# Kernel optimization log

Measured on AMD Instinct MI355X. Metric: run time of the kernel, lower is better.

Reference implementation:

```python
import jax, jax.numpy as jnp
import numpy as np

_SAMPLING_EPS = 1e-5
B, V = 256, 128000


def _apply_min_p(logits, min_p):
    # probs >= min_p * max_prob  <=>  keep; else logit -> -inf
    probs = jax.nn.softmax(logits, axis=-1)
    max_probs = jnp.max(probs, axis=-1, keepdims=True)
    keep = probs >= (min_p[:, None] * max_probs)
    return jnp.where(keep, logits, -jnp.inf)


def _apply_top_k_top_p(logits, top_k, top_p):
    # Sort ascending once; derive per-row keep-thresholds for both filters.
    logits_sort = jnp.sort(logits, axis=-1)  # [B, V] ascending
    # top-k threshold: value at position V-k (kth largest)
    k_idx = jnp.clip(V - top_k, 0, V - 1).astype(jnp.int32)
    k_thresh = jnp.take_along_axis(logits_sort, k_idx[:, None], axis=-1)  # [B,1]
    # top-p: on ascending-sorted probs, token is kept iff cumsum > 1 - p
    probs_sort = jax.nn.softmax(logits_sort, axis=-1)
    probs_cum = jnp.cumsum(probs_sort, axis=-1)
    kept = probs_cum > (1.0 - top_p[:, None])
    kept = kept.at[:, -1].set(True)  # always keep the max-prob token
    p_thresh = jnp.min(jnp.where(kept, logits_sort, jnp.inf), axis=-1, keepdims=True)
    thresh = jnp.maximum(k_thresh, p_thresh)
    return jnp.where(logits >= thresh, logits, -jnp.inf)


def setup_inputs() -> dict:
    key = jax.random.key(0)
    k1, k2, k3, k4, k5 = jax.random.split(key, 5)
    logits = jax.random.normal(k1, (B, V), jnp.float32)
    temperature = jax.random.uniform(k2, (B,), jnp.float32, 0.1, 1.5)
    temperature = temperature.at[:8].set(0.0)  # greedy rows
    min_p = jax.random.uniform(k3, (B,), jnp.float32, 0.0, 0.2)
    top_k = jax.random.randint(k4, (B,), 1, 64).astype(jnp.int32)
    top_p = jax.random.uniform(k5, (B,), jnp.float32, 0.5, 1.0)
    return {"logits": logits, "temperature": temperature, "min_p": min_p,
            "top_k": top_k, "top_p": top_p}


def reference(logits, temperature, min_p, top_k, top_p):
    logits = logits.astype(jnp.float32)
    greedy = jnp.argmax(logits, axis=-1)  # [B]
    # safe temperature divide (greedy rows have temp ~ 0 but are overridden)
    safe_t = jnp.where(temperature < _SAMPLING_EPS, 1.0, temperature)
    scaled = logits / safe_t[:, None]
    scaled = _apply_min_p(scaled, min_p)
    masked = _apply_top_k_top_p(scaled, top_k, top_p)
    # Gumbel-max trick == categorical sampling from softmax(masked)
    u = jax.random.uniform(jax.random.key(42), masked.shape, jnp.float32, 1e-10, 1.0)
    gumbel = -jnp.log(-jnp.log(u))
    random_sampled = jnp.argmax(masked + gumbel, axis=-1)
    sampled = jnp.where(temperature < _SAMPLING_EPS, greedy, random_sampled)
    return sampled[:, None]  # sampled_token_ids [B, 1]
```

## Files before the change

kernel.cpp:

```cpp
#include <hip/hip_runtime.h>
#include <stdint.h>

typedef unsigned long long u64;
typedef unsigned int u32;

#define VOCAB 128000
#define NV4   32000
#define NROWS 256
#define BLK   1024
#define NW    16
#define NB    4096
#define CAPL  4096
#define SEPS  1e-5f
#define FIXS  17592186044416.0

__device__ __forceinline__ u32 f2key(float f){
  u32 u = __float_as_uint(f);
  return (u & 0x80000000u) ? ~u : (u | 0x80000000u);
}
__device__ __forceinline__ float key2f(u32 k){
  u32 u = (k & 0x80000000u) ? (k ^ 0x80000000u) : ~k;
  return __uint_as_float(u);
}
__device__ __forceinline__ u64 efix(float e){
  return (u64)((double)e * FIXS);
}

__device__ __forceinline__ void tf2x32(u32 x0, u32 x1, u32 &o0, u32 &o1){
  const u32 k0 = 0u, k1 = 42u, k2 = 0u ^ 42u ^ 0x1BD11BDAu;
  x0 += k0; x1 += k1;
#define TFR(r) { x0 += x1; x1 = (x1 << (r)) | (x1 >> (32 - (r))); x1 ^= x0; }
  TFR(13) TFR(15) TFR(26) TFR(6)
  x0 += k1; x1 += k2 + 1u;
  TFR(17) TFR(29) TFR(16) TFR(24)
  x0 += k2; x1 += k0 + 2u;
  TFR(13) TFR(15) TFR(26) TFR(6)
  x0 += k0; x1 += k1 + 3u;
  TFR(17) TFR(29) TFR(16) TFR(24)
  x0 += k1; x1 += k2 + 4u;
  TFR(13) TFR(15) TFR(26) TFR(6)
  x0 += k2; x1 += k0 + 5u;
#undef TFR
  o0 = x0; o1 = x1;
}
__device__ __forceinline__ u32 gumbel_bits(u32 i){
  u32 o0, o1; tf2x32(0u, i, o0, o1);
  return o0 ^ o1;
}
__device__ __forceinline__ float bits2gumbel(u32 b){
  float f = __uint_as_float(0x3F800000u | (b >> 9)) - 1.0f;
  float u = fmaxf(1e-10f, f + 1e-10f);
  return -logf(-logf(u));
}

__device__ __forceinline__ void cross4096_u32(
    const u32* arr, u32* aux, u32 target, u32* out_idx, u32* out_before, int t)
{
  aux[t] = arr[4*t+0] + arr[4*t+1] + arr[4*t+2] + arr[4*t+3];
  __syncthreads();
  if (t < 64){
    u32 gs = 0u;
    #pragma unroll
    for (int j=0;j<16;j++) gs += aux[t*16+j];
    u32 pref = gs;
    #pragma unroll
    for (int d=1; d<64; d<<=1){ u32 v = __shfl_up(pref, d, 64); if (t >= d) pref += v; }
    u64 bal = __ballot(pref > target);
    int g = bal ? (__ffsll((long long)bal) - 1) : 63;
    u32 pg = __shfl(pref, g, 64);
    u32 gg = __shfl(gs, g, 64);
    if (t == 0){
      u32 c = pg - gg;
      u32 idx = (u32)(g*64 + 63);
      for (int j=0;j<16;j++){
        u32 v = aux[g*16+j];
        if (c + v > target){
          int base = (g*16+j)*4;
          for (int q=0;q<4;q++){
            u32 w = arr[base+q];
            if (c + w > target){ idx = (u32)(base+q); goto doneu; }
            c += w;
          }
        }
        c += v;
      }
      doneu:
      *out_idx = idx; *out_before = c;
    }
  }
}

__device__ __forceinline__ void cross4096_u64(
    const u64* arr, u64* aux, u64 target, u32* out_idx, u64* out_before, int t)
{
  aux[t] = arr[4*t+0] + arr[4*t+1] + arr[4*t+2] + arr[4*t+3];
  __syncthreads();
  if (t < 64){
    u64 gs = 0ull;
    #pragma unroll
    for (int j=0;j<16;j++) gs += aux[t*16+j];
    u64 pref = gs;
    #pragma unroll
    for (int d=1; d<64; d<<=1){
      u64 v = __shfl_up((unsigned long long)pref, d, 64); if (t >= d) pref += v;
    }
    u64 bal = __ballot(pref > target);
    int g = bal ? (__ffsll((long long)bal) - 1) : 63;
    u64 pg = __shfl((unsigned long long)pref, g, 64);
    u64 gg = __shfl((unsigned long long)gs, g, 64);
    if (t == 0){
      u64 c = pg - gg;
      u32 idx = (u32)(g*64 + 63);
      for (int j=0;j<16;j++){
        u64 v = aux[g*16+j];
        if (c + v > target){
          int base = (g*16+j)*4;
          for (int q=0;q<4;q++){
            u64 w = arr[base+q];
            if (c + w > target){ idx = (u32)(base+q); goto donev; }
            c += w;
          }
        }
        c += v;
      }
      donev:
      *out_idx = idx; *out_before = c;
    }
  }
}

__device__ __forceinline__ void cross4096_mass(
    const u64* arr, u64* aux, float topp_v, u64* out_target,
    u32* out_idx, u64* out_before, int t)
{
  aux[t] = arr[4*t+0] + arr[4*t+1] + arr[4*t+2] + arr[4*t+3];
  __syncthreads();
  if (t < 64){
    u64 gs = 0ull;
    #pragma unroll
    for (int j=0;j<16;j++) gs += aux[t*16+j];
    u64 pref = gs;
    #pragma unroll
    for (int d=1; d<64; d<<=1){
      u64 v = __shfl_up((unsigned long long)pref, d, 64); if (t >= d) pref += v;
    }
    u64 total = __shfl((unsigned long long)pref, 63, 64);
    u64 target = (u64)((double)(1.0f - topp_v) * (double)total);
    u64 bal = __ballot(pref > target);
    int g = bal ? (__ffsll((long long)bal) - 1) : 63;
    u64 pg = __shfl((unsigned long long)pref, g, 64);
    u64 gg = __shfl((unsigned long long)gs, g, 64);
    if (t == 0){
      u64 c = pg - gg;
      u32 idx = (u32)(g*64 + 63);
      for (int j=0;j<16;j++){
        u64 v = aux[g*16+j];
        if (c + v > target){
          int base = (g*16+j)*4;
          for (int q=0;q<4;q++){
            u64 w = arr[base+q];
            if (c + w > target){ idx = (u32)(base+q); goto donem; }
            c += w;
          }
        }
        c += v;
      }
      donem:
      *out_target = target; *out_idx = idx; *out_before = c;
    }
  }
}

__device__ __forceinline__ void cross256_u32(const u32* arr, u32 target, u32* out_idx, int t){
  if (t < 64){
    u32 gs = arr[4*t+0]+arr[4*t+1]+arr[4*t+2]+arr[4*t+3];
    u32 pref = gs;
    #pragma unroll
    for (int d=1; d<64; d<<=1){ u32 v=__shfl_up(pref,d,64); if (t>=d) pref+=v; }
    u64 bal = __ballot(pref > target);
    int g = bal ? (__ffsll((long long)bal)-1) : 63;
    u32 pg=__shfl(pref,g,64), gg=__shfl(gs,g,64);
    if (t==0){
      u32 c = pg-gg; u32 idx=(u32)(g*4+3);
      for (int q=0;q<4;q++){ u32 w=arr[g*4+q]; if (c+w>target){ idx=(u32)(g*4+q); break; } c+=w; }
      *out_idx = idx;
    }
  }
}
__device__ __forceinline__ void cross256_u64(const u64* arr, u64 target, u32* out_idx, int t){
  if (t < 64){
    u64 gs = arr[4*t+0]+arr[4*t+1]+arr[4*t+2]+arr[4*t+3];
    u64 pref = gs;
    #pragma unroll
    for (int d=1; d<64; d<<=1){
      u64 v=__shfl_up((unsigned long long)pref,d,64); if (t>=d) pref+=v;
    }
    u64 bal = __ballot(pref > target);
    int g = bal ? (__ffsll((long long)bal)-1) : 63;
    u64 pg=__shfl((unsigned long long)pref,g,64), gg=__shfl((unsigned long long)gs,g,64);
    if (t==0){
      u64 c = pg-gg; u32 idx=(u32)(g*4+3);
      for (int q=0;q<4;q++){ u64 w=arr[g*4+q]; if (c+w>target){ idx=(u32)(g*4+q); break; } c+=w; }
      *out_idx = idx;
    }
  }
}

__device__ __forceinline__ void msmerge(float &m1, float &S1, float m2, float S2){
  float mm = fmaxf(m1, m2);
  if (mm == -INFINITY){ m1 = mm; S1 = 0.0f; return; }
  S1 = S1*__expf(m1-mm) + S2*__expf(m2-mm);
  m1 = mm;
}

__device__ __forceinline__ void argmax_write(
    float best, u32 bi, float* wrf, u32* wru, int ln, int wv, int b, int* out)
{
  #pragma unroll
  for (int d=32; d>0; d>>=1){
    float c2=__shfl_down(best,d,64); u32 i2=__shfl_down(bi,d,64);
    if (c2>best || (c2==best && i2<bi)){best=c2;bi=i2;}
  }
  if (ln==0){ wrf[wv]=best; wru[wv]=bi; }
  __syncthreads();
  if (wv==0){
    float b1=(ln<NW)?wrf[ln]:-INFINITY; u32 i1=(ln<NW)?wru[ln]:0xFFFFFFFFu;
    #pragma unroll
    for (int d=32; d>0; d>>=1){
      float b2=__shfl_down(b1,d,64); u32 i2=__shfl_down(i1,d,64);
      if (b2>b1 || (b2==b1 && i2<i1)){b1=b2;i1=i2;}
    }
    if (ln==0) out[b]=(int)i1;
  }
}

__global__ __launch_bounds__(BLK) void k_all(
    const float* __restrict__ logits, const float* __restrict__ temp,
    const float* __restrict__ minp, const int* __restrict__ topk,
    const float* __restrict__ topp, int* __restrict__ out)
{
  __shared__ u32 cnt[NB];
  __shared__ u64 mass[NB];
  __shared__ u64 aux64[BLK];
  __shared__ u64 list[CAPL];
  __shared__ float wrf1[NW], wrf2[NW];
  __shared__ u32  wru1[NW];
  __shared__ float sh_m;
  __shared__ u32 sh_lstar, sh_K, sh_len, sh_acc1, sh_acc2;
  __shared__ u32 sh_idx, sh_bef32;
  __shared__ u64 sh_bef64, sh_tfix;

  u32* aux32 = (u32*)aux64;

  const int b = blockIdx.x;
  const int t = threadIdx.x;
  const int ln = t & 63, wv = t >> 6;
  const float T = temp[b];
  const float* row = logits + (size_t)b * VOCAB;
  const float4* row4 = (const float4*)row;

  if (T < SEPS){
    float M = -INFINITY; u32 Mi = 0xFFFFFFFFu;
    for (int i=t; i<NV4; i+=BLK){
      float4 q = row4[i];
      #pragma unroll
      for (int j=0;j<4;j++){
        float l = (&q.x)[j]; u32 gi = (u32)(i*4+j);
        if (l > M){ M = l; Mi = gi; }
      }
    }
    argmax_write(M, Mi, wrf1, wru1, ln, wv, b, out);
    return;
  }

  const float invT = 1.0f / T;
  for (int i=t;i<NB;i+=BLK) cnt[i]=0u;
  if (t==0){ sh_K=0u; sh_len=0u; sh_acc1=0u; sh_acc2=0u; }
  __syncthreads();
  float ms = -INFINITY, S = 0.0f;
  for (int i=t; i<NV4; i+=2*BLK){
    float4 qa = row4[i];
    int i2 = i + BLK;
    bool h2 = (i2 < NV4);
    float4 qb;
    if (h2) qb = row4[i2];
    #pragma unroll
    for (int j=0;j<4;j++){
      float l = (&qa.x)[j];
      float s = l * invT;
      if (s > ms){ S = S*__expf(ms - s) + 1.0f; ms = s; }
      else       { S += __expf(s - ms); }
      atomicAdd(&cnt[f2key(l)>>20], 1u);
    }
    if (h2){
      #pragma unroll
      for (int j=0;j<4;j++){
        float l = (&qb.x)[j];
        float s = l * invT;
        if (s > ms){ S = S*__expf(ms - s) + 1.0f; ms = s; }
        else       { S += __expf(s - ms); }
        atomicAdd(&cnt[f2key(l)>>20], 1u);
      }
    }
  }
  #pragma unroll
  for (int d=32; d>0; d>>=1){
    float m2 = __shfl_down(ms, d, 64); float S2 = __shfl_down(S, d, 64);
    msmerge(ms, S, m2, S2);
  }
  if (ln==0){ wrf1[wv]=ms; wrf2[wv]=S; }
  __syncthreads();
  if (wv==0){
    float m1 = (ln<NW)? wrf1[ln] : -INFINITY;
    float S1 = (ln<NW)? wrf2[ln] : 0.0f;
    #pragma unroll
    for (int d=32; d>0; d>>=1){
      float m2 = __shfl_down(m1, d, 64); float S2 = __shfl_down(S1, d, 64);
      msmerge(m1, S1, m2, S2);
    }
    if (ln==0){ sh_m = m1; wrf2[0] = S1; }
  }
  __syncthreads();
  const float m = sh_m, Z = wrf2[0];

  int tk = topk[b]; if (tk < 1) tk = 1; if (tk > VOCAB) tk = VOCAB;
  cross4096_u32(cnt, aux32, (u32)(VOCAB - tk), &sh_idx, &sh_bef32, t);
  __syncthreads();
  const u32 b1k = sh_idx;
  const u32 r1  = (u32)(VOCAB - tk + 1) - sh_bef32;

  if (t==0){
    float rhs = minp[b] * (1.0f / Z);
    u32 lo = 0u, hi = 0xFF800000u;
    while (lo < hi){
      u32 mid = lo + ((hi - lo) >> 1);
      float e = __expf(key2f(mid) * invT - m);
      if ((e / Z) >= rhs) hi = mid; else lo = mid + 1u;
    }
    sh_lstar = lo;
  }
  __syncthreads();
  const u32 lstar = sh_lstar;
  const u32 bl = lstar >> 20;

  {
    u32 pa=0u, pc=0u;
    for (int i=t;i<NB;i+=BLK){
      u32 c = cnt[i];
      if ((u32)i > bl)   pa += c;
      if ((u32)i >= b1k) pc += c;
    }
    #pragma unroll
    for (int d=32; d>0; d>>=1){ pa += __shfl_down(pa,d,64); pc += __shfl_down(pc,d,64); }
    if (ln==0){ atomicAdd(&sh_acc1, pa); atomicAdd(&sh_acc2, pc); }
  }
  __syncthreads();
  const u32 Kmin  = sh_acc1;
  const u32 cntbl = cnt[bl];
  const bool kcert = (Kmin >= (u32)tk);
  const u32 CLB = kcert ? b1k : bl;
  const u32 listlen = kcert ? sh_acc2 : (Kmin + cntbl);
  const bool fastOK = (listlen <= (u32)CAPL);

  for (int i=t;i<NB;i+=BLK) mass[i]=0ull;
  __syncthreads();
  u32 kc = 0u;
  for (int i=t; i<NV4; i+=2*BLK){
    float4 qa = row4[i];
    int i2 = i + BLK;
    bool h2 = (i2 < NV4);
    float4 qb;
    if (h2) qb = row4[i2];
    #pragma unroll
    for (int j=0;j<4;j++){
      float l = (&qa.x)[j];
      u32 key = f2key(l);
      if (key >= lstar){
        kc++;
        atomicAdd(&mass[key>>20], efix(__expf(l*invT - m)));
      }
      if (fastOK && (key>>20) >= CLB){
        u32 p = atomicAdd(&sh_len, 1u);
        list[p] = ((u64)key << 32) | (u64)(u32)(i*4+j);
      }
    }
    if (h2){
      #pragma unroll
      for (int j=0;j<4;j++){
        float l = (&qb.x)[j];
        u32 key = f2key(l);
        if (key >= lstar){
          kc++;
          atomicAdd(&mass[key>>20], efix(__expf(l*invT - m)));
        }
        if (fastOK && (key>>20) >= CLB){
          u32 p = atomicAdd(&sh_len, 1u);
          list[p] = ((u64)key << 32) | (u64)(u32)(i2*4+j);
        }
      }
    }
  }
  #pragma unroll
  for (int d=32; d>0; d>>=1) kc += __shfl_down(kc, d, 64);
  if (ln==0) atomicAdd(&sh_K, kc);
  __syncthreads();
  const u32 K = sh_K;
  const bool kval = (K >= (u32)tk);
  cross4096_mass(mass, aux64, topp[b], &sh_tfix, &sh_idx, &sh_bef64, t);
  __syncthreads();
  const u32 b1p = sh_idx;
  const u64 t1  = sh_tfix - sh_bef64;
  const u32 llen = sh_len;
  const bool needK = kval && (b1p <= b1k);
  const bool needP = (!kval) || (b1p >= b1k);

  u32 kkey = 0u, pkey = 0u;

  if (fastOK){
    if (needK){
      for (int i=t;i<NB;i+=BLK) cnt[i]=0u;
      __syncthreads();
      for (u32 i=t; i<llen; i+=BLK){
        u32 key = (u32)(list[i]>>32);
        if ((key>>20) == b1k) atomicAdd(&cnt[(key>>8)&0xFFFu], 1u);
      }
      __syncthreads();
      cross4096_u32(cnt, aux32, r1-1u, &sh_idx, &sh_bef32, t);
      __syncthreads();
      u32 b2k = sh_idx, r2 = r1 - sh_bef32;
      u32 prefk = (b1k<<12) | b2k;
      for (int i=t;i<256;i+=BLK) cnt[i]=0u;
      __syncthreads();
      for (u32 i=t; i<llen; i+=BLK){
        u32 key = (u32)(list[i]>>32);
        if ((key>>8) == prefk) atomicAdd(&cnt[key&0xFFu], 1u);
      }
      __syncthreads();
      cross256_u32(cnt, r2-1u, &sh_idx, t);
      __syncthreads();
      kkey = (prefk<<8) | sh_idx;
    }
    if (needP){
      for (int i=t;i<NB;i+=BLK) mass[i]=0ull;
      __syncthreads();
      for (u32 i=t; i<llen; i+=BLK){
        u32 key = (u32)(list[i]>>32);
        if ((key>>20) == b1p && key >= lstar)
          atomicAdd(&mass[(key>>8)&0xFFFu], efix(__expf(key2f(key)*invT - m)));
      }
      __syncthreads();
      cross4096_u64(mass, aux64, t1, &sh_idx, &sh_bef64, t);
      __syncthreads();
      u32 b2p = sh_idx; u64 t2 = t1 - sh_bef64;
      u32 prefp = (b1p<<12) | b2p;
      for (int i=t;i<256;i+=BLK) mass[i]=0ull;
      __syncthreads();
      for (u32 i=t; i<llen; i+=BLK){
        u32 key = (u32)(list[i]>>32);
        if ((key>>8) == prefp && key >= lstar)
          atomicAdd(&mass[key&0xFFu], efix(__expf(key2f(key)*invT - m)));
      }
      __syncthreads();
      cross256_u64(mass, t2, &sh_idx, t);
      __syncthreads();
      pkey = (prefp<<8) | sh_idx;
    }
    const u32 thrkey = kkey > pkey ? kkey : pkey;

    float best = -INFINITY; u32 bi = 0xFFFFFFFFu;
    for (u32 i=t; i<llen; i+=BLK){
      u64 e = list[i];
      u32 key = (u32)(e>>32);
      if (key >= thrkey){
        u32 idx = (u32)e;
        u32 c = (u32)b * (u32)VOCAB + idx;
        float cand = key2f(key)*invT + bits2gumbel(gumbel_bits(c));
        if (cand > best || (cand == best && idx < bi)){ best = cand; bi = idx; }
      }
    }
    argmax_write(best, bi, wrf1, wru1, ln, wv, b, out);
    return;
  }

  for (int i=t;i<NB;i+=BLK){ cnt[i]=0u; mass[i]=0ull; }
  __syncthreads();
  for (int i=t; i<NV4; i+=BLK){
    float4 q = row4[i];
    #pragma unroll
    for (int j=0;j<4;j++){
      float l = (&q.x)[j]; u32 key = f2key(l); u32 hi = key>>20;
      if (kval && hi == b1k) atomicAdd(&cnt[(key>>8)&0xFFFu], 1u);
      if (hi == b1p && key >= lstar)
        atomicAdd(&mass[(key>>8)&0xFFFu], efix(__expf(l*invT - m)));
    }
  }
  __syncthreads();
  cross4096_u32(cnt, aux32, r1-1u, &sh_idx, &sh_bef32, t);
  __syncthreads();
  u32 b2k = sh_idx, r2 = r1 - sh_bef32;
  cross4096_u64(mass, aux64, t1, &sh_idx, &sh_bef64, t);
  __syncthreads();
  u32 b2p = sh_idx; u64 t2 = t1 - sh_bef64;
  for (int i=t;i<256;i+=BLK){ cnt[i]=0u; mass[i]=0ull; }
  __syncthreads();
  for (int i=t; i<NV4; i+=BLK){
    float4 q = row4[i];
    #pragma unroll
    for (int j=0;j<4;j++){
      float l = (&q.x)[j]; u32 key = f2key(l);
      if (kval && (key>>8)==(((b1k<<12)|b2k)))
        atomicAdd(&cnt[key&0xFFu], 1u);
      if ((key>>8)==(((b1p<<12)|b2p)) && key >= lstar)
        atomicAdd(&mass[key&0xFFu], efix(__expf(l*invT - m)));
    }
  }
  __syncthreads();
  cross256_u32(cnt, r2-1u, &sh_idx, t);
  __syncthreads();
  if (kval) kkey = (b1k<<20)|(b2k<<8)|sh_idx;
  cross256_u64(mass, t2, &sh_idx, t);
  __syncthreads();
  pkey = (b1p<<20)|(b2p<<8)|sh_idx;
  const float thrf = key2f(kkey > pkey ? kkey : pkey);

  float best = -INFINITY; u32 bi = 0xFFFFFFFFu;
  for (int i=t; i<NV4; i+=BLK){
    float4 q = row4[i];
    #pragma unroll
    for (int j=0;j<4;j++){
      float l = (&q.x)[j];
      if (l >= thrf){
        u32 idx = (u32)(i*4+j);
        u32 c = (u32)b * (u32)VOCAB + idx;
        float cand = l*invT + bits2gumbel(gumbel_bits(c));
        if (cand > best || (cand == best && idx < bi)){ best = cand; bi = idx; }
      }
    }
  }
  argmax_write(best, bi, wrf1, wru1, ln, wv, b, out);
}

extern "C" void kernel_launch(void* const* d_in, const int* in_sizes, int n_in,
                              void* d_out, int out_size, void* d_ws, size_t ws_size,
                              hipStream_t stream)
{
  const float* logits = (const float*)d_in[0];
  const float* temp   = (const float*)d_in[1];
  const float* minp   = (const float*)d_in[2];
  const int*   topk   = (const int*)d_in[3];
  const float* topp   = (const float*)d_in[4];
  int* out = (int*)d_out;

  hipLaunchKernelGGL(k_all, dim3(NROWS), dim3(BLK), 0, stream,
                     logits, temp, minp, topk, topp, out);
}
```

Measured before the change: 63.93 us.

## Compute per-bucket exp mass in first pass and drop online softmax

The first pass now tracks only the row max, and per top bucket it accumulates exp mass measured relative to each bucket's lower edge. The global normalizer Z and the kept mass are then rebuilt in double precision by rescaling each bucket with exp(edge*invT - m). This removes the online-softmax rescaling and the second full mass histogram in the middle pass, which now only accumulates mass for the boundary bucket. It adds a second 64-bit shared atomic in the first pass plus several tree reductions. It also risks precision differences from the per-bucket fixed-point scaling.

```diff
diff --git a/kernel.cpp b/kernel.cpp
--- a/kernel.cpp
+++ b/kernel.cpp
@@ -1,5 +1,6 @@
 #include <hip/hip_runtime.h>
 #include <stdint.h>
+#include <math.h>
 
 typedef unsigned long long u64;
 typedef unsigned int u32;
@@ -12,7 +13,6 @@
 #define NB    4096
 #define CAPL  4096
 #define SEPS  1e-5f
-#define FIXS  17592186044416.0
 
 __device__ __forceinline__ u32 f2key(float f){
   u32 u = __float_as_uint(f);
@@ -22,8 +22,12 @@
   u32 u = (k & 0x80000000u) ? (k ^ 0x80000000u) : ~k;
   return __uint_as_float(u);
 }
-__device__ __forceinline__ u64 efix(float e){
-  return (u64)((double)e * FIXS);
+__device__ __forceinline__ u64 localm(float l, float edge, float invT){
+  return (u64)(__expf((l - edge) * invT) * 1.099511627776e12f);
+}
+__device__ __forceinline__ double scaleb(u32 b, double invTd, double md){
+  double e = (double)key2f(b << 20);
+  return exp(e * invTd - md) * 9.094947017729282e-13;
 }
 
 __device__ __forceinline__ void tf2x32(u32 x0, u32 x1, u32 &o0, u32 &o1){
@@ -129,44 +133,41 @@
   }
 }
 
-__device__ __forceinline__ void cross4096_mass(
-    const u64* arr, u64* aux, float topp_v, u64* out_target,
-    u32* out_idx, u64* out_before, int t)
+__device__ __forceinline__ void cross4096_f64(
+    const double* arr, double* aux, double target, u32* out_idx, double* out_before, int t)
 {
   aux[t] = arr[4*t+0] + arr[4*t+1] + arr[4*t+2] + arr[4*t+3];
   __syncthreads();
   if (t < 64){
-    u64 gs = 0ull;
+    double gs = 0.0;
     #pragma unroll
     for (int j=0;j<16;j++) gs += aux[t*16+j];
-    u64 pref = gs;
+    double pref = gs;
     #pragma unroll
     for (int d=1; d<64; d<<=1){
-      u64 v = __shfl_up((unsigned long long)pref, d, 64); if (t >= d) pref += v;
-    }
-    u64 total = __shfl((unsigned long long)pref, 63, 64);
-    u64 target = (u64)((double)(1.0f - topp_v) * (double)total);
+      double v = __shfl_up(pref, d, 64); if (t >= d) pref += v;
+    }
     u64 bal = __ballot(pref > target);
     int g = bal ? (__ffsll((long long)bal) - 1) : 63;
-    u64 pg = __shfl((unsigned long long)pref, g, 64);
-    u64 gg = __shfl((unsigned long long)gs, g, 64);
+    double pg = __shfl(pref, g, 64);
+    double gg = __shfl(gs, g, 64);
     if (t == 0){
-      u64 c = pg - gg;
+      double c = pg - gg;
       u32 idx = (u32)(g*64 + 63);
       for (int j=0;j<16;j++){
-        u64 v = aux[g*16+j];
+        double v = aux[g*16+j];
         if (c + v > target){
           int base = (g*16+j)*4;
           for (int q=0;q<4;q++){
-            u64 w = arr[base+q];
-            if (c + w > target){ idx = (u32)(base+q); goto donem; }
+            double w = arr[base+q];
+            if (c + w > target){ idx = (u32)(base+q); goto donef; }
             c += w;
           }
         }
         c += v;
       }
-      donem:
-      *out_target = target; *out_idx = idx; *out_before = c;
+      donef:
+      *out_idx = idx; *out_before = c;
     }
   }
 }
@@ -206,13 +207,6 @@
   }
 }
 
-__device__ __forceinline__ void msmerge(float &m1, float &S1, float m2, float S2){
-  float mm = fmaxf(m1, m2);
-  if (mm == -INFINITY){ m1 = mm; S1 = 0.0f; return; }
-  S1 = S1*__expf(m1-mm) + S2*__expf(m2-mm);
-  m1 = mm;
-}
-
 __device__ __forceinline__ void argmax_write(
     float best, u32 bi, float* wrf, u32* wru, int ln, int wv, int b, int* out)
 {
@@ -240,17 +234,20 @@
     const float* __restrict__ topp, int* __restrict__ out)
 {
   __shared__ u32 cnt[NB];
-  __shared__ u64 mass[NB];
+  __shared__ u64 lmass[NB];
+  __shared__ u64 list[CAPL];
   __shared__ u64 aux64[BLK];
-  __shared__ u64 list[CAPL];
-  __shared__ float wrf1[NW], wrf2[NW];
-  __shared__ u32  wru1[NW];
-  __shared__ float sh_m;
-  __shared__ u32 sh_lstar, sh_K, sh_len, sh_acc1, sh_acc2;
-  __shared__ u32 sh_idx, sh_bef32;
-  __shared__ u64 sh_bef64, sh_tfix;
+  __shared__ float wrf[NW];
+  __shared__ u32  wru[NW];
+  __shared__ u64  wrull[NW];
+  __shared__ float sh_maxL, sh_Z32;
+  __shared__ u32 sh_lstar, sh_len, sh_idx, sh_bef32, sh_u1, sh_u2;
+  __shared__ u64 sh_bef64, sh_km;
+  __shared__ double sh_befd, sh_Md;
 
   u32* aux32 = (u32*)aux64;
+  double* auxd = (double*)aux64;
+  double* absd = (double*)lmass;
 
   const int b = blockIdx.x;
   const int t = threadIdx.x;
@@ -269,59 +266,68 @@
         if (l > M){ M = l; Mi = gi; }
       }
     }
-    argmax_write(M, Mi, wrf1, wru1, ln, wv, b, out);
+    argmax_write(M, Mi, wrf, wru, ln, wv, b, out);
     return;
   }
 
   const float invT = 1.0f / T;
-  for (int i=t;i<NB;i+=BLK) cnt[i]=0u;
-  if (t==0){ sh_K=0u; sh_len=0u; sh_acc1=0u; sh_acc2=0u; }
-  __syncthreads();
-  float ms = -INFINITY, S = 0.0f;
-  for (int i=t; i<NV4; i+=2*BLK){
-    float4 qa = row4[i];
-    int i2 = i + BLK;
-    bool h2 = (i2 < NV4);
-    float4 qb;
-    if (h2) qb = row4[i2];
-    #pragma unroll
-    for (int j=0;j<4;j++){
-      float l = (&qa.x)[j];
-      float s = l * invT;
-      if (s > ms){ S = S*__expf(ms - s) + 1.0f; ms = s; }
-      else       { S += __expf(s - ms); }
-      atomicAdd(&cnt[f2key(l)>>20], 1u);
-    }
-    if (h2){
+
+  for (int i=t;i<NB;i+=BLK){ cnt[i]=0u; lmass[i]=0ull; }
+  if (t==0){ sh_len = 0u; }
+  __syncthreads();
+  {
+    float mx = -INFINITY;
+    for (int i=t; i<NV4; i+=2*BLK){
+      float4 qa = row4[i];
+      int i2 = i + BLK; bool h2 = (i2 < NV4);
+      float4 qb; if (h2) qb = row4[i2];
       #pragma unroll
       for (int j=0;j<4;j++){
-        float l = (&qb.x)[j];
-        float s = l * invT;
-        if (s > ms){ S = S*__expf(ms - s) + 1.0f; ms = s; }
-        else       { S += __expf(s - ms); }
-        atomicAdd(&cnt[f2key(l)>>20], 1u);
-      }
-    }
-  }
-  #pragma unroll
-  for (int d=32; d>0; d>>=1){
-    float m2 = __shfl_down(ms, d, 64); float S2 = __shfl_down(S, d, 64);
-    msmerge(ms, S, m2, S2);
-  }
-  if (ln==0){ wrf1[wv]=ms; wrf2[wv]=S; }
-  __syncthreads();
-  if (wv==0){
-    float m1 = (ln<NW)? wrf1[ln] : -INFINITY;
-    float S1 = (ln<NW)? wrf2[ln] : 0.0f;
-    #pragma unroll
-    for (int d=32; d>0; d>>=1){
-      float m2 = __shfl_down(m1, d, 64); float S2 = __shfl_down(S1, d, 64);
-      msmerge(m1, S1, m2, S2);
-    }
-    if (ln==0){ sh_m = m1; wrf2[0] = S1; }
-  }
-  __syncthreads();
-  const float m = sh_m, Z = wrf2[0];
+        float l = (&qa.x)[j];
+        mx = fmaxf(mx, l);
+        u32 key = f2key(l); u32 bk = key >> 20;
+        atomicAdd(&cnt[bk], 1u);
+        atomicAdd(&lmass[bk], localm(l, key2f(bk<<20), invT));
+      }
+      if (h2){
+        #pragma unroll
+        for (int j=0;j<4;j++){
+          float l = (&qb.x)[j];
+          mx = fmaxf(mx, l);
+          u32 key = f2key(l); u32 bk = key >> 20;
+          atomicAdd(&cnt[bk], 1u);
+          atomicAdd(&lmass[bk], localm(l, key2f(bk<<20), invT));
+        }
+      }
+    }
+    #pragma unroll
+    for (int d=32; d>0; d>>=1) mx = fmaxf(mx, __shfl_down(mx, d, 64));
+    if (ln==0) wrf[wv] = mx;
+    __syncthreads();
+    if (t==0){
+      float m1 = wrf[0];
+      for (int w=1; w<NW; w++) m1 = fmaxf(m1, wrf[w]);
+      sh_maxL = m1;
+    }
+  }
+  __syncthreads();
+  const float m = sh_maxL * invT;
+  const double invTd = (double)invT, md = (double)m;
+
+  for (int i0=t*4; i0<(t+1)*4; i0++){
+    u64 lm = lmass[i0];
+    double a = lm ? ((double)lm * scaleb((u32)i0, invTd, md)) : 0.0;
+    absd[i0] = a;
+  }
+  __syncthreads();
+  {
+    double s = absd[4*t+0]+absd[4*t+1]+absd[4*t+2]+absd[4*t+3];
+    auxd[t] = s; __syncthreads();
+    for (int off=512; off>0; off>>=1){ if (t<off) auxd[t] += auxd[t+off]; __syncthreads(); }
+    if (t==0) sh_Z32 = (float)auxd[0];
+    __syncthreads();
+  }
+  const float Z = sh_Z32;
 
   int tk = topk[b]; if (tk < 1) tk = 1; if (tk > VOCAB) tk = VOCAB;
   cross4096_u32(cnt, aux32, (u32)(VOCAB - tk), &sh_idx, &sh_bef32, t);
@@ -344,75 +350,96 @@
   const u32 bl = lstar >> 20;
 
   {
-    u32 pa=0u, pc=0u;
-    for (int i=t;i<NB;i+=BLK){
-      u32 c = cnt[i];
-      if ((u32)i > bl)   pa += c;
-      if ((u32)i >= b1k) pc += c;
-    }
-    #pragma unroll
-    for (int d=32; d>0; d>>=1){ pa += __shfl_down(pa,d,64); pc += __shfl_down(pc,d,64); }
-    if (ln==0){ atomicAdd(&sh_acc1, pa); atomicAdd(&sh_acc2, pc); }
-  }
-  __syncthreads();
-  const u32 Kmin  = sh_acc1;
-  const u32 cntbl = cnt[bl];
+    u32 pa = 0u;
+    for (int i=t;i<NB;i+=BLK) if ((u32)i > bl) pa += cnt[i];
+    aux32[t] = pa; __syncthreads();
+    for (int off=512; off>0; off>>=1){ if (t<off) aux32[t] += aux32[t+off]; __syncthreads(); }
+    if (t==0) sh_u1 = aux32[0];
+    __syncthreads();
+  }
+  const u32 Kmin = sh_u1;
   const bool kcert = (Kmin >= (u32)tk);
   const u32 CLB = kcert ? b1k : bl;
-  const u32 listlen = kcert ? sh_acc2 : (Kmin + cntbl);
+  {
+    u32 pa = 0u;
+    for (int i=t;i<NB;i+=BLK) if ((u32)i >= CLB) pa += cnt[i];
+    aux32[t] = pa; __syncthreads();
+    for (int off=512; off>0; off>>=1){ if (t<off) aux32[t] += aux32[t+off]; __syncthreads(); }
+    if (t==0) sh_u2 = aux32[0];
+    __syncthreads();
+  }
+  const u32 listlen = sh_u2;
   const bool fastOK = (listlen <= (u32)CAPL);
-
-  for (int i=t;i<NB;i+=BLK) mass[i]=0ull;
-  __syncthreads();
-  u32 kc = 0u;
-  for (int i=t; i<NV4; i+=2*BLK){
-    float4 qa = row4[i];
-    int i2 = i + BLK;
-    bool h2 = (i2 < NV4);
-    float4 qb;
-    if (h2) qb = row4[i2];
-    #pragma unroll
-    for (int j=0;j<4;j++){
-      float l = (&qa.x)[j];
-      u32 key = f2key(l);
-      if (key >= lstar){
-        kc++;
-        atomicAdd(&mass[key>>20], efix(__expf(l*invT - m)));
-      }
-      if (fastOK && (key>>20) >= CLB){
-        u32 p = atomicAdd(&sh_len, 1u);
-        list[p] = ((u64)key << 32) | (u64)(u32)(i*4+j);
-      }
-    }
-    if (h2){
+  const float edgebl = key2f(bl << 20);
+
+  {
+    u32 kc = 0u; u64 km = 0ull;
+    for (int i=t; i<NV4; i+=2*BLK){
+      float4 qa = row4[i];
+      int i2 = i + BLK; bool h2 = (i2 < NV4);
+      float4 qb; if (h2) qb = row4[i2];
       #pragma unroll
       for (int j=0;j<4;j++){
-        float l = (&qb.x)[j];
-        u32 key = f2key(l);
-        if (key >= lstar){
-          kc++;
-          atomicAdd(&mass[key>>20], efix(__expf(l*invT - m)));
+        float l = (&qa.x)[j];
+        u32 key = f2key(l); u32 bk = key >> 20;
+        if (fastOK && bk >= CLB){
+          u32 p = atomicAdd(&sh_len, 1u);
+          if (p < CAPL) list[p] = ((u64)key << 32) | (u64)(u32)(i*4+j);
         }
-        if (fastOK && (key>>20) >= CLB){
-          u32 p = atomicAdd(&sh_len, 1u);
-          list[p] = ((u64)key << 32) | (u64)(u32)(i2*4+j);
+        if (bk == bl && key >= lstar){ kc++; km += localm(l, edgebl, invT); }
+      }
+      if (h2){
+        #pragma unroll
+        for (int j=0;j<4;j++){
+          float l = (&qb.x)[j];
+          u32 key = f2key(l); u32 bk = key >> 20;
+          if (fastOK && bk >= CLB){
+            u32 p = atomicAdd(&sh_len, 1u);
+            if (p < CAPL) list[p] = ((u64)key << 32) | (u64)(u32)(i2*4+j);
+          }
+          if (bk == bl && key >= lstar){ kc++; km += localm(l, edgebl, invT); }
         }
       }
     }
-  }
-  #pragma unroll
-  for (int d=32; d>0; d>>=1) kc += __shfl_down(kc, d, 64);
-  if (ln==0) atomicAdd(&sh_K, kc);
-  __syncthreads();
-  const u32 K = sh_K;
+    #pragma unroll
+    for (int d=32; d>0; d>>=1){
+      kc += __shfl_down(kc, d, 64);
+      km += __shfl_down((unsigned long long)km, d, 64);
+    }
+    if (ln==0){ wru[wv] = kc; wrull[wv] = km; }
+    __syncthreads();
+    if (t==0){
+      u32 K = Kmin; u64 kmt = 0ull;
+      for (int w=0; w<NW; w++){ K += wru[w]; kmt += wrull[w]; }
+      sh_u1 = K; sh_km = kmt;
+    }
+    __syncthreads();
+  }
+  const u32 K = sh_u1;
   const bool kval = (K >= (u32)tk);
-  cross4096_mass(mass, aux64, topp[b], &sh_tfix, &sh_idx, &sh_bef64, t);
+  const u32 llen = sh_len;
+
+  for (int i=t;i<NB;i+=BLK) if ((u32)i < bl) absd[i] = 0.0;
+  if (t==0) absd[bl] = sh_km ? ((double)sh_km * scaleb(bl, invTd, md)) : 0.0;
+  __syncthreads();
+  {
+    double s = absd[4*t+0]+absd[4*t+1]+absd[4*t+2]+absd[4*t+3];
+    auxd[t] = s; __syncthreads();
+    for (int off=512; off>0; off>>=1){ if (t<off) auxd[t] += auxd[t+off]; __syncthreads(); }
+    if (t==0) sh_Md = auxd[0];
+    __syncthreads();
+  }
+  const double Mkept = sh_Md;
+  const double tp = (double)(1.0f - topp[b]) * Mkept;
+  cross4096_f64(absd, auxd, tp, &sh_idx, &sh_befd, t);
   __syncthreads();
   const u32 b1p = sh_idx;
-  const u64 t1  = sh_tfix - sh_bef64;
-  const u32 llen = sh_len;
+  const double t1 = tp - sh_befd;
   const bool needK = kval && (b1p <= b1k);
   const bool needP = (!kval) || (b1p >= b1k);
+  const double scp = scaleb(b1p, invTd, md);
+  const u64 t1u = (u64)(t1 / scp);
+  const float edgep = key2f(b1p << 20);
 
   u32 kkey = 0u, pkey = 0u;
 
@@ -441,27 +468,27 @@
       kkey = (prefk<<8) | sh_idx;
     }
     if (needP){
-      for (int i=t;i<NB;i+=BLK) mass[i]=0ull;
+      for (int i=t;i<NB;i+=BLK) lmass[i]=0ull;
       __syncthreads();
       for (u32 i=t; i<llen; i+=BLK){
         u32 key = (u32)(list[i]>>32);
         if ((key>>20) == b1p && key >= lstar)
-          atomicAdd(&mass[(key>>8)&0xFFFu], efix(__expf(key2f(key)*invT - m)));
-      }
-      __syncthreads();
-      cross4096_u64(mass, aux64, t1, &sh_idx, &sh_bef64, t);
-      __syncthreads();
-      u32 b2p = sh_idx; u64 t2 = t1 - sh_bef64;
+          atomicAdd(&lmass[(key>>8)&0xFFFu], localm(key2f(key), edgep, invT));
+      }
+      __syncthreads();
+      cross4096_u64(lmass, aux64, t1u, &sh_idx, &sh_bef64, t);
+      __syncthreads();
+      u32 b2p = sh_idx; u64 t2u = t1u - sh_bef64;
       u32 prefp = (b1p<<12) | b2p;
-      for (int i=t;i<256;i+=BLK) mass[i]=0ull;
+      for (int i=t;i<256;i+=BLK) lmass[i]=0ull;
       __syncthreads();
       for (u32 i=t; i<llen; i+=BLK){
         u32 key = (u32)(list[i]>>32);
         if ((key>>8) == prefp && key >= lstar)
-          atomicAdd(&mass[key&0xFFu], efix(__expf(key2f(key)*invT - m)));
-      }
-      __syncthreads();
-      cross256_u64(mass, t2, &sh_idx, t);
+          atomicAdd(&lmass[key&0xFFu], localm(key2f(key), edgep, invT));
+      }
+      __syncthreads();
+      cross256_u64(lmass, t2u, &sh_idx, t);
       __syncthreads();
       pkey = (prefp<<8) | sh_idx;
     }
@@ -478,51 +505,60 @@
         if (cand > best || (cand == best && idx < bi)){ best = cand; bi = idx; }
       }
     }
-    argmax_write(best, bi, wrf1, wru1, ln, wv, b, out);
+    argmax_write(best, bi, wrf, wru, ln, wv, b, out);
     return;
   }
 
-  for (int i=t;i<NB;i+=BLK){ cnt[i]=0u; mass[i]=0ull; }
+  for (int i=t;i<NB;i+=BLK){ cnt[i]=0u; lmass[i]=0ull; }
   __syncthreads();
   for (int i=t; i<NV4; i+=BLK){
     float4 q = row4[i];
     #pragma unroll
     for (int j=0;j<4;j++){
-      float l = (&q.x)[j]; u32 key = f2key(l); u32 hi = key>>20;
-      if (kval && hi == b1k) atomicAdd(&cnt[(key>>8)&0xFFFu], 1u);
-      if (hi == b1p && key >= lstar)
-        atomicAdd(&mass[(key>>8)&0xFFFu], efix(__expf(l*invT - m)));
-    }
-  }
-  __syncthreads();
-  cross4096_u32(cnt, aux32, r1-1u, &sh_idx, &sh_bef32, t);
-  __syncthreads();
-  u32 b2k = sh_idx, r2 = r1 - sh_bef32;
-  cross4096_u64(mass, aux64, t1, &sh_idx, &sh_bef64, t);
-  __syncthreads();
-  u32 b2p = sh_idx; u64 t2 = t1 - sh_bef64;
-  for (int i=t;i<256;i+=BLK){ cnt[i]=0u; mass[i]=0ull; }
+      float l = (&q.x)[j]; u32 key = f2key(l); u32 bk = key>>20;
+      if (needK && bk == b1k) atomicAdd(&cnt[(key>>8)&0xFFFu], 1u);
+      if (needP && bk == b1p && key >= lstar)
+        atomicAdd(&lmass[(key>>8)&0xFFFu], localm(l, edgep, invT));
+    }
+  }
+  __syncthreads();
+  u32 b2k = 0u, r2 = 1u, b2p = 0u; u64 t2u = 0ull;
+  if (needK){
+    cross4096_u32(cnt, aux32, r1-1u, &sh_idx, &sh_bef32, t);
+    __syncthreads();
+    b2k = sh_idx; r2 = r1 - sh_bef32;
+  }
+  if (needP){
+    cross4096_u64(lmass, aux64, t1u, &sh_idx, &sh_bef64, t);
+    __syncthreads();
+    b2p = sh_idx; t2u = t1u - sh_bef64;
+  }
+  const u32 prefk = (b1k<<12) | b2k;
+  const u32 prefp = (b1p<<12) | b2p;
+  for (int i=t;i<256;i+=BLK){ cnt[i]=0u; lmass[i]=0ull; }
   __syncthreads();
   for (int i=t; i<NV4; i+=BLK){
     float4 q = row4[i];
     #pragma unroll
     for (int j=0;j<4;j++){
       float l = (&q.x)[j]; u32 key = f2key(l);
-      if (kval && (key>>8)==(((b1k<<12)|b2k)))
-        atomicAdd(&cnt[key&0xFFu], 1u);
-      if ((key>>8)==(((b1p<<12)|b2p)) && key >= lstar)
-        atomicAdd(&mass[key&0xFFu], efix(__expf(l*invT - m)));
-    }
-  }
-  __syncthreads();
-  cross256_u32(cnt, r2-1u, &sh_idx, t);
-  __syncthreads();
-  if (kval) kkey = (b1k<<20)|(b2k<<8)|sh_idx;
-  cross256_u64(mass, t2, &sh_idx, t);
-  __syncthreads();
-  pkey = (b1p<<20)|(b2p<<8)|sh_idx;
+      if (needK && (key>>8) == prefk) atomicAdd(&cnt[key&0xFFu], 1u);
+      if (needP && (key>>8) == prefp && key >= lstar)
+        atomicAdd(&lmass[key&0xFFu], localm(l, edgep, invT));
+    }
+  }
+  __syncthreads();
+  if (needK){
+    cross256_u32(cnt, r2-1u, &sh_idx, t);
+    __syncthreads();
+    kkey = (prefk<<8) | sh_idx;
+  }
+  if (needP){
+    cross256_u64(lmass, t2u, &sh_idx, t);
+    __syncthreads();
+    pkey = (prefp<<8) | sh_idx;
+  }
   const float thrf = key2f(kkey > pkey ? kkey : pkey);
-
   float best = -INFINITY; u32 bi = 0xFFFFFFFFu;
   for (int i=t; i<NV4; i+=BLK){
     float4 q = row4[i];
@@ -537,7 +573,7 @@
       }
     }
   }
-  argmax_write(best, bi, wrf1, wru1, ln, wv, b, out);
+  argmax_write(best, bi, wrf, wru, ln, wv, b, out);
 }
 
 extern "C" void kernel_launch(void* const* d_in, const int* in_sizes, int n_in,
```

Result: slower. 71.36 us (+11.6%).

## Use exp-scaled fixed-point mass, split accumulators, and wave-parallel min-p search

Applied to the files above, without the earlier changes.

Folds the 2^40 fixed-point scale into the exponent (exp(x+40 ln2)) so the double-precision multiply and convert are dropped. The mass histogram is split by thread parity to cut LDS atomic contention, and four independent online-softmax accumulators break the serial dependency chain. The single-thread binary search for the min-p threshold becomes a 64-way ballot search across one wave, and block reductions go through per-wave slots instead of shared atomics. The fallback path also skips the k or p refinement when it is not needed. Risks are slightly different rounding in the fixed-point mass and higher LDS use from the doubled mass array.

```diff
diff --git a/kernel.cpp b/kernel.cpp
--- a/kernel.cpp
+++ b/kernel.cpp
@@ -12,7 +12,7 @@
 #define NB    4096
 #define CAPL  4096
 #define SEPS  1e-5f
-#define FIXS  17592186044416.0
+#define LN2X40 27.725887222397812f
 
 __device__ __forceinline__ u32 f2key(float f){
   u32 u = __float_as_uint(f);
@@ -21,9 +21,6 @@
 __device__ __forceinline__ float key2f(u32 k){
   u32 u = (k & 0x80000000u) ? (k ^ 0x80000000u) : ~k;
   return __uint_as_float(u);
-}
-__device__ __forceinline__ u64 efix(float e){
-  return (u64)((double)e * FIXS);
 }
 
 __device__ __forceinline__ void tf2x32(u32 x0, u32 x1, u32 &o0, u32 &o1){
@@ -240,14 +237,13 @@
     const float* __restrict__ topp, int* __restrict__ out)
 {
   __shared__ u32 cnt[NB];
-  __shared__ u64 mass[NB];
+  __shared__ u64 massI[2*NB];
+  __shared__ u64 list[CAPL];
   __shared__ u64 aux64[BLK];
-  __shared__ u64 list[CAPL];
   __shared__ float wrf1[NW], wrf2[NW];
-  __shared__ u32  wru1[NW];
-  __shared__ float sh_m;
-  __shared__ u32 sh_lstar, sh_K, sh_len, sh_acc1, sh_acc2;
-  __shared__ u32 sh_idx, sh_bef32;
+  __shared__ u32  wru1[NW], wru2[NW];
+  __shared__ float sh_m, sh_Z;
+  __shared__ u32 sh_lstar, sh_len, sh_idx, sh_bef32, sh_u1, sh_u2, sh_u3;
   __shared__ u64 sh_bef64, sh_tfix;
 
   u32* aux32 = (u32*)aux64;
@@ -275,53 +271,50 @@
 
   const float invT = 1.0f / T;
   for (int i=t;i<NB;i+=BLK) cnt[i]=0u;
-  if (t==0){ sh_K=0u; sh_len=0u; sh_acc1=0u; sh_acc2=0u; }
-  __syncthreads();
-  float ms = -INFINITY, S = 0.0f;
+  for (int i=t;i<2*NB;i+=BLK) massI[i]=0ull;
+  if (t==0) sh_len=0u;
+  __syncthreads();
+
+  float ms0=-INFINITY,S0=0.0f, ms1=-INFINITY,S1=0.0f,
+        ms2=-INFINITY,S2=0.0f, ms3=-INFINITY,S3=0.0f;
+#define ONLINE(LV, MS, SS) { \
+    float l_ = (LV); \
+    atomicAdd(&cnt[f2key(l_)>>20], 1u); \
+    float s_ = l_ * invT; \
+    float d_ = s_ - MS; \
+    float e_ = __expf(-fabsf(d_)); \
+    if (d_ > 0.0f){ SS = fmaf(SS, e_, 1.0f); MS = s_; } else { SS += e_; } \
+  }
   for (int i=t; i<NV4; i+=2*BLK){
     float4 qa = row4[i];
-    int i2 = i + BLK;
-    bool h2 = (i2 < NV4);
-    float4 qb;
-    if (h2) qb = row4[i2];
-    #pragma unroll
-    for (int j=0;j<4;j++){
-      float l = (&qa.x)[j];
-      float s = l * invT;
-      if (s > ms){ S = S*__expf(ms - s) + 1.0f; ms = s; }
-      else       { S += __expf(s - ms); }
-      atomicAdd(&cnt[f2key(l)>>20], 1u);
-    }
+    int i2 = i + BLK; bool h2 = (i2 < NV4);
+    float4 qb; if (h2) qb = row4[i2];
+    ONLINE(qa.x,ms0,S0) ONLINE(qa.y,ms1,S1) ONLINE(qa.z,ms2,S2) ONLINE(qa.w,ms3,S3)
     if (h2){
-      #pragma unroll
-      for (int j=0;j<4;j++){
-        float l = (&qb.x)[j];
-        float s = l * invT;
-        if (s > ms){ S = S*__expf(ms - s) + 1.0f; ms = s; }
-        else       { S += __expf(s - ms); }
-        atomicAdd(&cnt[f2key(l)>>20], 1u);
-      }
-    }
-  }
+      ONLINE(qb.x,ms0,S0) ONLINE(qb.y,ms1,S1) ONLINE(qb.z,ms2,S2) ONLINE(qb.w,ms3,S3)
+    }
+  }
+#undef ONLINE
+  msmerge(ms0,S0,ms1,S1); msmerge(ms2,S2,ms3,S3); msmerge(ms0,S0,ms2,S2);
   #pragma unroll
   for (int d=32; d>0; d>>=1){
-    float m2 = __shfl_down(ms, d, 64); float S2 = __shfl_down(S, d, 64);
-    msmerge(ms, S, m2, S2);
-  }
-  if (ln==0){ wrf1[wv]=ms; wrf2[wv]=S; }
+    float mz = __shfl_down(ms0, d, 64); float Sz = __shfl_down(S0, d, 64);
+    msmerge(ms0, S0, mz, Sz);
+  }
+  if (ln==0){ wrf1[wv]=ms0; wrf2[wv]=S0; }
   __syncthreads();
   if (wv==0){
     float m1 = (ln<NW)? wrf1[ln] : -INFINITY;
-    float S1 = (ln<NW)? wrf2[ln] : 0.0f;
+    float Sx = (ln<NW)? wrf2[ln] : 0.0f;
     #pragma unroll
     for (int d=32; d>0; d>>=1){
-      float m2 = __shfl_down(m1, d, 64); float S2 = __shfl_down(S1, d, 64);
-      msmerge(m1, S1, m2, S2);
-    }
-    if (ln==0){ sh_m = m1; wrf2[0] = S1; }
-  }
-  __syncthreads();
-  const float m = sh_m, Z = wrf2[0];
+      float mz=__shfl_down(m1,d,64); float Sz=__shfl_down(Sx,d,64);
+      msmerge(m1, Sx, mz, Sz);
+    }
+    if (ln==0){ sh_m = m1; sh_Z = Sx; }
+  }
+  __syncthreads();
+  const float m = sh_m, Z = sh_Z;
 
   int tk = topk[b]; if (tk < 1) tk = 1; if (tk > VOCAB) tk = VOCAB;
   cross4096_u32(cnt, aux32, (u32)(VOCAB - tk), &sh_idx, &sh_bef32, t);
@@ -329,15 +322,27 @@
   const u32 b1k = sh_idx;
   const u32 r1  = (u32)(VOCAB - tk + 1) - sh_bef32;
 
-  if (t==0){
-    float rhs = minp[b] * (1.0f / Z);
+  if (wv==0){
+    const float rhs = minp[b] * (1.0f / Z);
     u32 lo = 0u, hi = 0xFF800000u;
-    while (lo < hi){
-      u32 mid = lo + ((hi - lo) >> 1);
-      float e = __expf(key2f(mid) * invT - m);
-      if ((e / Z) >= rhs) hi = mid; else lo = mid + 1u;
-    }
-    sh_lstar = lo;
+    while (hi - lo > 64u){
+      u32 step = (hi - lo) >> 6;
+      u32 k = lo + (u32)(ln + 1) * step;
+      float e = __expf(fmaf(key2f(k), invT, -m));
+      u64 bal = __ballot((e / Z) >= rhs);
+      if (bal){
+        u32 g = (u32)(__ffsll((long long)bal) - 1);
+        hi = lo + (g + 1u) * step;
+        lo = lo + g * step;
+      } else {
+        lo += 64u * step;
+      }
+    }
+    u32 k = lo + 1u + (u32)ln;
+    bool ok = (k <= hi);
+    float e = __expf(fmaf(key2f(k), invT, -m));
+    u64 bal = __ballot(ok && ((e / Z) >= rhs));
+    if (ln==0) sh_lstar = bal ? (lo + 1u + (u32)(__ffsll((long long)bal) - 1)) : hi;
   }
   __syncthreads();
   const u32 lstar = sh_lstar;
@@ -352,65 +357,67 @@
     }
     #pragma unroll
     for (int d=32; d>0; d>>=1){ pa += __shfl_down(pa,d,64); pc += __shfl_down(pc,d,64); }
-    if (ln==0){ atomicAdd(&sh_acc1, pa); atomicAdd(&sh_acc2, pc); }
-  }
-  __syncthreads();
-  const u32 Kmin  = sh_acc1;
-  const u32 cntbl = cnt[bl];
+    if (ln==0){ wru1[wv]=pa; wru2[wv]=pc; }
+    __syncthreads();
+    if (t==0){
+      u32 a=0u, c2=0u;
+      for (int w=0; w<NW; w++){ a += wru1[w]; c2 += wru2[w]; }
+      sh_u1 = a; sh_u2 = c2;
+    }
+    __syncthreads();
+  }
+  const u32 Kmin = sh_u1;
   const bool kcert = (Kmin >= (u32)tk);
   const u32 CLB = kcert ? b1k : bl;
-  const u32 listlen = kcert ? sh_acc2 : (Kmin + cntbl);
+  const u32 listlen = kcert ? sh_u2 : (Kmin + cnt[bl]);
   const bool fastOK = (listlen <= (u32)CAPL);
-
-  for (int i=t;i<NB;i+=BLK) mass[i]=0ull;
-  __syncthreads();
+  const float cs = LN2X40 - m;
+
   u32 kc = 0u;
+#define P2E(LV, IDX) { \
+    float l_ = (LV); u32 key_ = f2key(l_); u32 bk_ = key_ >> 20; \
+    if (key_ >= lstar){ \
+      kc++; \
+      u64 lm_ = (u64)__expf(fmaf(l_, invT, cs)); \
+      if (lm_) atomicAdd(&massI[(bk_<<1) | (u32)(t&1)], lm_); \
+    } \
+    if (fastOK && bk_ >= CLB){ \
+      u32 p_ = atomicAdd(&sh_len, 1u); \
+      if (p_ < CAPL) list[p_] = ((u64)key_ << 32) | (u64)(u32)(IDX); \
+    } \
+  }
   for (int i=t; i<NV4; i+=2*BLK){
     float4 qa = row4[i];
-    int i2 = i + BLK;
-    bool h2 = (i2 < NV4);
-    float4 qb;
-    if (h2) qb = row4[i2];
-    #pragma unroll
-    for (int j=0;j<4;j++){
-      float l = (&qa.x)[j];
-      u32 key = f2key(l);
-      if (key >= lstar){
-        kc++;
-        atomicAdd(&mass[key>>20], efix(__expf(l*invT - m)));
-      }
-      if (fastOK && (key>>20) >= CLB){
-        u32 p = atomicAdd(&sh_len, 1u);
-        list[p] = ((u64)key << 32) | (u64)(u32)(i*4+j);
-      }
-    }
+    int i2 = i + BLK; bool h2 = (i2 < NV4);
+    float4 qb; if (h2) qb = row4[i2];
+    P2E(qa.x, i*4+0) P2E(qa.y, i*4+1) P2E(qa.z, i*4+2) P2E(qa.w, i*4+3)
     if (h2){
-      #pragma unroll
-      for (int j=0;j<4;j++){
-        float l = (&qb.x)[j];
-        u32 key = f2key(l);
-        if (key >= lstar){
-          kc++;
-          atomicAdd(&mass[key>>20], efix(__expf(l*invT - m)));
-        }
-        if (fastOK && (key>>20) >= CLB){
-          u32 p = atomicAdd(&sh_len, 1u);
-          list[p] = ((u64)key << 32) | (u64)(u32)(i2*4+j);
-        }
-      }
-    }
-  }
+      P2E(qb.x, i2*4+0) P2E(qb.y, i2*4+1) P2E(qb.z, i2*4+2) P2E(qb.w, i2*4+3)
+    }
+  }
+#undef P2E
   #pragma unroll
   for (int d=32; d>0; d>>=1) kc += __shfl_down(kc, d, 64);
-  if (ln==0) atomicAdd(&sh_K, kc);
-  __syncthreads();
-  const u32 K = sh_K;
+  if (ln==0) wru1[wv] = kc;
+  __syncthreads();
+  if (t==0){ u32 K2=0u; for (int w=0;w<NW;w++) K2 += wru1[w]; sh_u3 = K2; }
+  {
+    u64 g0 = massI[8*t+0] + massI[8*t+1];
+    u64 g1 = massI[8*t+2] + massI[8*t+3];
+    u64 g2 = massI[8*t+4] + massI[8*t+5];
+    u64 g3 = massI[8*t+6] + massI[8*t+7];
+    __syncthreads();
+    massI[4*t+0]=g0; massI[4*t+1]=g1; massI[4*t+2]=g2; massI[4*t+3]=g3;
+  }
+  __syncthreads();
+  const u32 K = sh_u3;
   const bool kval = (K >= (u32)tk);
-  cross4096_mass(mass, aux64, topp[b], &sh_tfix, &sh_idx, &sh_bef64, t);
+  const u32 llen = sh_len;
+
+  cross4096_mass(massI, aux64, topp[b], &sh_tfix, &sh_idx, &sh_bef64, t);
   __syncthreads();
   const u32 b1p = sh_idx;
   const u64 t1  = sh_tfix - sh_bef64;
-  const u32 llen = sh_len;
   const bool needK = kval && (b1p <= b1k);
   const bool needP = (!kval) || (b1p >= b1k);
 
@@ -441,27 +448,31 @@
       kkey = (prefk<<8) | sh_idx;
     }
     if (needP){
-      for (int i=t;i<NB;i+=BLK) mass[i]=0ull;
+      for (int i=t;i<NB;i+=BLK) massI[i]=0ull;
       __syncthreads();
       for (u32 i=t; i<llen; i+=BLK){
         u32 key = (u32)(list[i]>>32);
-        if ((key>>20) == b1p && key >= lstar)
-          atomicAdd(&mass[(key>>8)&0xFFFu], efix(__expf(key2f(key)*invT - m)));
-      }
-      __syncthreads();
-      cross4096_u64(mass, aux64, t1, &sh_idx, &sh_bef64, t);
+        if ((key>>20) == b1p && key >= lstar){
+          u64 lm = (u64)__expf(fmaf(key2f(key), invT, cs));
+          if (lm) atomicAdd(&massI[(key>>8)&0xFFFu], lm);
+        }
+      }
+      __syncthreads();
+      cross4096_u64(massI, aux64, t1, &sh_idx, &sh_bef64, t);
       __syncthreads();
       u32 b2p = sh_idx; u64 t2 = t1 - sh_bef64;
       u32 prefp = (b1p<<12) | b2p;
-      for (int i=t;i<256;i+=BLK) mass[i]=0ull;
+      for (int i=t;i<256;i+=BLK) massI[i]=0ull;
       __syncthreads();
       for (u32 i=t; i<llen; i+=BLK){
         u32 key = (u32)(list[i]>>32);
-        if ((key>>8) == prefp && key >= lstar)
-          atomicAdd(&mass[key&0xFFu], efix(__expf(key2f(key)*invT - m)));
-      }
-      __syncthreads();
-      cross256_u64(mass, t2, &sh_idx, t);
+        if ((key>>8) == prefp && key >= lstar){
+          u64 lm = (u64)__expf(fmaf(key2f(key), invT, cs));
+          if (lm) atomicAdd(&massI[key&0xFFu], lm);
+        }
+      }
+      __syncthreads();
+      cross256_u64(massI, t2, &sh_idx, t);
       __syncthreads();
       pkey = (prefp<<8) | sh_idx;
     }
@@ -482,47 +493,60 @@
     return;
   }
 
-  for (int i=t;i<NB;i+=BLK){ cnt[i]=0u; mass[i]=0ull; }
+  for (int i=t;i<NB;i+=BLK){ cnt[i]=0u; massI[i]=0ull; }
   __syncthreads();
   for (int i=t; i<NV4; i+=BLK){
     float4 q = row4[i];
     #pragma unroll
     for (int j=0;j<4;j++){
-      float l = (&q.x)[j]; u32 key = f2key(l); u32 hi = key>>20;
-      if (kval && hi == b1k) atomicAdd(&cnt[(key>>8)&0xFFFu], 1u);
-      if (hi == b1p && key >= lstar)
-        atomicAdd(&mass[(key>>8)&0xFFFu], efix(__expf(l*invT - m)));
-    }
-  }
-  __syncthreads();
-  cross4096_u32(cnt, aux32, r1-1u, &sh_idx, &sh_bef32, t);
-  __syncthreads();
-  u32 b2k = sh_idx, r2 = r1 - sh_bef32;
-  cross4096_u64(mass, aux64, t1, &sh_idx, &sh_bef64, t);
-  __syncthreads();
-  u32 b2p = sh_idx; u64 t2 = t1 - sh_bef64;
-  for (int i=t;i<256;i+=BLK){ cnt[i]=0u; mass[i]=0ull; }
+      float l = (&q.x)[j]; u32 key = f2key(l); u32 hb = key>>20;
+      if (needK && hb == b1k) atomicAdd(&cnt[(key>>8)&0xFFFu], 1u);
+      if (needP && hb == b1p && key >= lstar){
+        u64 lm = (u64)__expf(fmaf(l, invT, cs));
+        if (lm) atomicAdd(&massI[(key>>8)&0xFFFu], lm);
+      }
+    }
+  }
+  __syncthreads();
+  u32 b2k = 0u, r2 = 1u, b2p = 0u; u64 t2 = 0ull;
+  if (needK){
+    cross4096_u32(cnt, aux32, r1-1u, &sh_idx, &sh_bef32, t);
+    __syncthreads();
+    b2k = sh_idx; r2 = r1 - sh_bef32;
+  }
+  if (needP){
+    cross4096_u64(massI, aux64, t1, &sh_idx, &sh_bef64, t);
+    __syncthreads();
+    b2p = sh_idx; t2 = t1 - sh_bef64;
+  }
+  const u32 prefk = (b1k<<12) | b2k;
+  const u32 prefp = (b1p<<12) | b2p;
+  for (int i=t;i<256;i+=BLK){ cnt[i]=0u; massI[i]=0ull; }
   __syncthreads();
   for (int i=t; i<NV4; i+=BLK){
     float4 q = row4[i];
     #pragma unroll
     for (int j=0;j<4;j++){
       float l = (&q.x)[j]; u32 key = f2key(l);
-      if (kval && (key>>8)==(((b1k<<12)|b2k)))
-        atomicAdd(&cnt[key&0xFFu], 1u);
-      if ((key>>8)==(((b1p<<12)|b2p)) && key >= lstar)
-        atomicAdd(&mass[key&0xFFu], efix(__expf(l*invT - m)));
-    }
-  }
-  __syncthreads();
-  cross256_u32(cnt, r2-1u, &sh_idx, t);
-  __syncthreads();
-  if (kval) kkey = (b1k<<20)|(b2k<<8)|sh_idx;
-  cross256_u64(mass, t2, &sh_idx, t);
-  __syncthreads();
-  pkey = (b1p<<20)|(b2p<<8)|sh_idx;
+      if (needK && (key>>8) == prefk) atomicAdd(&cnt[key&0xFFu], 1u);
+      if (needP && (key>>8) == prefp && key >= lstar){
+        u64 lm = (u64)__expf(fmaf(l, invT, cs));
+        if (lm) atomicAdd(&massI[key&0xFFu], lm);
+      }
+    }
+  }
+  __syncthreads();
+  if (needK){
+    cross256_u32(cnt, r2-1u, &sh_idx, t);
+    __syncthreads();
+    kkey = (prefk<<8) | sh_idx;
+  }
+  if (needP){
+    cross256_u64(massI, t2, &sh_idx, t);
+    __syncthreads();
+    pkey = (prefp<<8) | sh_idx;
+  }
   const float thrf = key2f(kkey > pkey ? kkey : pkey);
-
   float best = -INFINITY; u32 bi = 0xFFFFFFFFu;
   for (int i=t; i<NV4; i+=BLK){
     float4 q = row4[i];
```

After: 60.18 us. 5.9% less time.
